# Optimization experiments

Measured on AMD Instinct MI355X. Metric: run time of the kernel, lower is better.

Reference implementation:

```python
import jax, jax.numpy as jnp
import numpy as np
import math

B, S, E, H = 4, 1024, 1024, 16
HD = E // H
MAX_SEQ = 5000
THETA = 10000.0


def _freqs_cis():
    # RotaryPositionalEncoding buffer: complex64 [MAX_SEQ, E//2]
    freqs = 1.0 / (THETA ** (np.arange(0, E, 2)[: E // 2] / E))
    ang = np.outer(np.arange(MAX_SEQ), freqs)
    return jnp.asarray(np.exp(1j * ang).astype(np.complex64))


def _rope(x, idx, fc_table):
    # x: [B, S, E]; pairs consecutive channels across the FULL embed_dim
    # (applied before head splitting, faithful to the original module)
    xc = x.reshape(*x.shape[:-1], -1, 2)
    xc = jax.lax.complex(xc[..., 0], xc[..., 1])  # [B, S, E//2]
    out = xc * fc_table[idx]                       # [B, S, E//2]
    return jnp.stack([jnp.real(out), jnp.imag(out)], axis=-1).reshape(x.shape)


def reference(query, key, value, query_index, key_index, attn_mask,
              key_padding_mask, Wq, bq, Wk, bk, Wv, bv, Wo, bo):
    q = query @ Wq.T + bq
    k = key @ Wk.T + bk
    v = value @ Wv.T + bv

    fc = _freqs_cis()
    q = _rope(q, query_index, fc)
    k = _rope(k, key_index, fc)

    # torch: q = cat(q.chunk(H, dim=-1), dim=0) -> flat HEAD-MAJOR [H*B, S, HD]
    qf = q.reshape(B, S, H, HD).transpose(2, 0, 1, 3).reshape(H * B, S, HD)
    kf = k.reshape(B, S, H, HD).transpose(2, 0, 1, 3).reshape(H * B, S, HD)
    vf = v.reshape(B, S, H, HD).transpose(2, 0, 1, 3).reshape(H * B, S, HD)

    # mask: logical_or(attn_mask[Sq,Sk], kpm[B,1,Sk]) -> [B, Sq, Sk]
    m = jnp.logical_or(attn_mask[None, :, :], key_padding_mask[:, None, :])
    madd = jnp.where(m, -jnp.inf, 0.0).astype(query.dtype)
    # torch repeat_interleave(H, dim=0) yields BATCH-MAJOR flat [B*H, Sq, Sk];
    # it is added to the head-major scores as-is (faithful to the original
    # indexing, including its head/batch-order quirk)
    madd_flat = jnp.repeat(madd, H, axis=0)

    scores = jnp.einsum('nqd,nkd->nqk', qf / math.sqrt(HD), kf) + madd_flat
    w = jax.nn.softmax(scores, axis=-1)              # [H*B, Sq, Sk]
    of = jnp.einsum('nqk,nkd->nqd', w, vf)           # [H*B, Sq, HD]

    # cat(chunks(dim=0), dim=-1) -> [B, Sq, E], head-major last dim
    attn_output = of.reshape(H, B, S, HD).transpose(1, 2, 0, 3).reshape(B, S, E)
    attn_output = attn_output @ Wo.T + bo

    # stack(chunks(dim=0), dim=1).mean(1) -> [B, Sq, Sk]
    attn_weights = w.reshape(H, B, S, S).transpose(1, 0, 2, 3).mean(axis=1)
    return attn_output, attn_weights


def setup_inputs() -> dict:
    key0 = jax.random.key(0)
    ks = jax.random.split(key0, 10)
    sc = 0.02
    inp = {
        'query': jax.random.normal(ks[0], (B, S, E), jnp.float32),
        'key': jax.random.normal(ks[1], (B, S, E), jnp.float32),
        'value': jax.random.normal(ks[2], (B, S, E), jnp.float32),
        'query_index': jnp.sort(jax.random.randint(ks[3], (B, S), 0, 4096), axis=-1),
        'key_index': jnp.sort(jax.random.randint(ks[4], (B, S), 0, 4096), axis=-1),
        'attn_mask': jnp.triu(jnp.ones((S, S), jnp.bool_), k=1),  # causal
        'key_padding_mask': jnp.zeros((B, S), jnp.bool_),
        'Wq': jax.random.normal(ks[5], (E, E), jnp.float32) * sc,
        'bq': jnp.zeros((E,), jnp.float32),
        'Wk': jax.random.normal(ks[6], (E, E), jnp.float32) * sc,
        'bk': jnp.zeros((E,), jnp.float32),
        'Wv': jax.random.normal(ks[7], (E, E), jnp.float32) * sc,
        'bv': jnp.zeros((E,), jnp.float32),
        'Wo': jax.random.normal(ks[8], (E, E), jnp.float32) * sc,
        'bo': jnp.zeros((E,), jnp.float32),
    }
    return inp
```

## Files before the change

### kernel.cpp

```cpp
#include <hip/hip_runtime.h>
#include <stdint.h>
#include <math.h>

#define B_ 4
#define S_ 1024
#define E_ 1024
#define H_ 16
#define HD_ 64
#define HB_ 64

typedef __attribute__((ext_vector_type(8))) short bhalf8;
typedef __attribute__((ext_vector_type(4))) float floatx4;

__device__ __forceinline__ unsigned short f2bf(float f) {
  union { float f; unsigned u; } v; v.f = f;
  unsigned r = (v.u + 0x7FFFu + ((v.u >> 16) & 1u)) >> 16;
  return (unsigned short)r;
}
__device__ __forceinline__ float bf2f(unsigned short b) {
  union { unsigned u; float f; } v; v.u = ((unsigned)b) << 16;
  return v.f;
}
__device__ __forceinline__ unsigned cvtpk_bf16(float a, float b) {
  unsigned r;
  asm volatile("v_cvt_pk_bf16_f32 %0, %1, %2" : "=v"(r) : "v"(a), "v"(b));
  return r;
}

__device__ __forceinline__ void gload16(const void* g, void* l) {
  __builtin_amdgcn_global_load_lds(
      (const __attribute__((address_space(1))) unsigned int*)g,
      (__attribute__((address_space(3))) unsigned int*)l, 16, 0, 0);
}

template <int NCH>
__device__ __forceinline__ void stage_tile(const unsigned short* org,
                                           unsigned short* lds, int wave, int lane) {
  const int rl = lane >> 3;
  const int scb = ((lane & 7) << 4) ^ (rl << 4);
  const char* base = (const char*)org + scb;
#pragma unroll
  for (int i = 0; i < NCH / 4; ++i) {
    const int c = wave + 4 * i;
    gload16(base + (size_t)(c * 8 + rl) * 2048, (char*)lds + c * 1024);
  }
}

__device__ __forceinline__ bhalf8 read_frag(const unsigned short* lds, int row, int kbyte) {
  const int off = row * 128 + (kbyte ^ ((row & 7) << 4));
  return *(const bhalf8*)((const char*)lds + off);
}

__global__ void detect_bool_kernel(const uint8_t* __restrict__ amask, int* __restrict__ flag) {
  if (threadIdx.x == 0 && blockIdx.x == 0) *flag = (amask[1] != 0) ? 1 : 0;
}

__global__ __launch_bounds__(256) void mprep_kernel(
    const void* __restrict__ amask, const void* __restrict__ kpm,
    const int* __restrict__ flagp, unsigned long long* __restrict__ Mbits) {
  const int gid = blockIdx.x * 256 + threadIdx.x;
  const int word = gid & 15, q = (gid >> 4) & 1023, bp = gid >> 14;
  const int k0 = word * 64;
  unsigned long long bits = 0;
  if (*flagp) {
    const uint8_t* ap = (const uint8_t*)amask + (size_t)q * 1024 + k0;
    const uint8_t* kp = (const uint8_t*)kpm + (size_t)bp * 1024 + k0;
#pragma unroll
    for (int c = 0; c < 4; ++c) {
      uint4 a = *(const uint4*)(ap + c * 16);
      uint4 k = *(const uint4*)(kp + c * 16);
      unsigned aw[4] = {a.x | k.x, a.y | k.y, a.z | k.z, a.w | k.w};
#pragma unroll
      for (int wv = 0; wv < 4; ++wv)
#pragma unroll
        for (int bt = 0; bt < 4; ++bt)
          if ((aw[wv] >> (8 * bt)) & 0xffu)
            bits |= 1ull << (c * 16 + wv * 4 + bt);
    }
  } else {
    const int* ap = (const int*)amask + (size_t)q * 1024 + k0;
    const int* kp = (const int*)kpm + (size_t)bp * 1024 + k0;
#pragma unroll
    for (int c = 0; c < 16; ++c) {
      int4 a = *(const int4*)(ap + c * 4);
      int4 k = *(const int4*)(kp + c * 4);
      if (a.x | k.x) bits |= 1ull << (c * 4 + 0);
      if (a.y | k.y) bits |= 1ull << (c * 4 + 1);
      if (a.z | k.z) bits |= 1ull << (c * 4 + 2);
      if (a.w | k.w) bits |= 1ull << (c * 4 + 3);
    }
  }
  Mbits[((size_t)bp << 14) + (size_t)q * 16 + word] = bits;
}

__global__ __launch_bounds__(256) void cvt_all_kernel(
    const float* __restrict__ q, const float* __restrict__ k,
    const float* __restrict__ v,
    const float* __restrict__ wq, const float* __restrict__ wk,
    const float* __restrict__ wv, const float* __restrict__ wo,
    unsigned short* __restrict__ Ab, unsigned short* __restrict__ Wb) {
  const int z = blockIdx.z;
  if (z >= 3 && blockIdx.x >= 512) return;
  const float* src;
  unsigned short* dst;
  if (z < 3) {
    src = (z == 0) ? q : (z == 1) ? k : v;
    dst = Ab + (size_t)z * 4194304;
  } else {
    const int zz = z - 3;
    src = (zz == 0) ? wq : (zz == 1) ? wk : (zz == 2) ? wv : wo;
    dst = Wb + (size_t)zz * 1048576;
  }
  const size_t i = ((size_t)blockIdx.x * 256 + threadIdx.x) * 8;
  float4 a = *(const float4*)(src + i);
  float4 b = *(const float4*)(src + i + 4);
  bhalf8 r;
  r[0] = (short)f2bf(a.x); r[1] = (short)f2bf(a.y);
  r[2] = (short)f2bf(a.z); r[3] = (short)f2bf(a.w);
  r[4] = (short)f2bf(b.x); r[5] = (short)f2bf(b.y);
  r[6] = (short)f2bf(b.z); r[7] = (short)f2bf(b.w);
  *(bhalf8*)(dst + i) = r;
}

template <bool QKV>
__global__ __launch_bounds__(256) void mfma_gemm_kernel(
    const unsigned short* __restrict__ A0, const unsigned short* __restrict__ A1,
    const unsigned short* __restrict__ A2,
    const unsigned short* __restrict__ W0, const unsigned short* __restrict__ W1,
    const unsigned short* __restrict__ W2,
    const float* __restrict__ b0, const float* __restrict__ b1,
    const float* __restrict__ b2,
    void* __restrict__ C0, void* __restrict__ C1, void* __restrict__ C2) {
  const int nb = gridDim.z * 256;
  const int chunk = nb >> 3;
  const int g = blockIdx.z * 256 + blockIdx.y * 8 + blockIdx.x;
  const int swz = (g & 7) * chunk + (g >> 3);
  const int zt = swz >> 8;
  const int r8 = swz & 255;
  const int m0 = (r8 >> 3) * 128, n0 = (r8 & 7) * 128;
  const unsigned short* A = (zt == 0) ? A0 : (zt == 1) ? A1 : A2;
  const unsigned short* W = (zt == 0) ? W0 : (zt == 1) ? W1 : W2;
  const float* bias = (zt == 0) ? b0 : (zt == 1) ? b1 : b2;
  void* C = (zt == 0) ? C0 : (zt == 1) ? C1 : C2;
  __shared__ unsigned short As[128 * 64];
  __shared__ unsigned short Ws[128 * 64];
  const int t = threadIdx.x, wave = t >> 6, lane = t & 63;
  const int wr = wave >> 1, wc = wave & 1;
  const int l4 = lane >> 4, l15 = lane & 15;
  floatx4 acc[4][4];
  const floatx4 z4 = {0.f, 0.f, 0.f, 0.f};
#pragma unroll
  for (int i = 0; i < 4; ++i)
#pragma unroll
    for (int j = 0; j < 4; ++j) acc[i][j] = z4;

  for (int k0 = 0; k0 < 1024; k0 += 64) {
    stage_tile<16>(A + (size_t)m0 * 1024 + k0, As, wave, lane);
    stage_tile<16>(W + (size_t)n0 * 1024 + k0, Ws, wave, lane);
    __syncthreads();
#pragma unroll
    for (int ks = 0; ks < 2; ++ks) {
      const int kb = ks * 64 + (l4 << 4);
      bhalf8 af[4], bf[4];
#pragma unroll
      for (int mi = 0; mi < 4; ++mi)
        af[mi] = read_frag(As, wr * 64 + mi * 16 + l15, kb);
#pragma unroll
      for (int ni = 0; ni < 4; ++ni)
        bf[ni] = read_frag(Ws, wc * 64 + ni * 16 + l15, kb);
#pragma unroll
      for (int mi = 0; mi < 4; ++mi)
#pragma unroll
        for (int ni = 0; ni < 4; ++ni)
          acc[mi][ni] = __builtin_amdgcn_mfma_f32_16x16x32_bf16(af[mi], bf[ni], acc[mi][ni], 0, 0, 0);
    }
    __syncthreads();
  }

  if (QKV && zt == 2) {
#pragma unroll
    for (int mi = 0; mi < 4; ++mi) {
      const int row0 = m0 + wr * 64 + mi * 16 + l4 * 4;
      const int b = row0 >> 10, s = row0 & 1023;
#pragma unroll
      for (int ni = 0; ni < 4; ++ni) {
        const int col = n0 + wc * 64 + ni * 16 + l15;
        const int h = col >> 6, d = col & 63;
        const float bv = bias[col];
        ushort4 o;
        o.x = f2bf(acc[mi][ni][0] + bv);
        o.y = f2bf(acc[mi][ni][1] + bv);
        o.z = f2bf(acc[mi][ni][2] + bv);
        o.w = f2bf(acc[mi][ni][3] + bv);
        *(ushort4*)((unsigned short*)C +
                    (((size_t)(b * 16 + h) * 64 + d) << 10) + s) = o;
      }
    }
  } else {
#pragma unroll
    for (int mi = 0; mi < 4; ++mi)
#pragma unroll
      for (int ni = 0; ni < 4; ++ni) {
        const int col = n0 + wc * 64 + ni * 16 + l15;
        const float bv = bias[col];
#pragma unroll
        for (int r = 0; r < 4; ++r) {
          const int row = m0 + wr * 64 + mi * 16 + l4 * 4 + r;
          const float v = acc[mi][ni][r] + bv;
          if (QKV)
            ((unsigned short*)C)[(size_t)row * 1024 + col] = f2bf(v);
          else
            ((float*)C)[(size_t)row * 1024 + col] = v;
        }
      }
  }
}

__global__ __launch_bounds__(256) void rope_bf_kernel(
    unsigned int* __restrict__ Q, unsigned int* __restrict__ K,
    const int* __restrict__ qidx, const int* __restrict__ kidx) {
  const int z = blockIdx.y;
  unsigned int* X = z ? K : Q;
  const int* idxs = z ? kidx : qidx;
  const int gid = blockIdx.x * 256 + threadIdx.x;
  const int i = gid & 511, bs = gid >> 9;
  const int pos = idxs[bs];
  const float fr = exp2f((float)i * (-13.287712379549449f / 512.0f));
  const float ang = (float)pos * fr;
  float sn, c;
  sincosf(ang, &sn, &c);
  const unsigned v = X[gid];
  const float x = bf2f((unsigned short)(v & 0xffffu));
  const float y = bf2f((unsigned short)(v >> 16));
  const float rx = x * c - y * sn;
  const float ry = x * sn + y * c;
  X[gid] = (unsigned)f2bf(rx) | ((unsigned)f2bf(ry) << 16);
}

__global__ __launch_bounds__(256) void scores_sm_kernel(
    const unsigned short* __restrict__ Qr, const unsigned short* __restrict__ Kr,
    unsigned short* __restrict__ P, const unsigned long long* __restrict__ Mbits,
    int hb0, int nwg) {
  const int lin = blockIdx.y * 64 + blockIdx.x;
  const int q8 = nwg >> 3;
  const int swz = (lin & 7) * q8 + (lin >> 3);
  const int qb = swz & 63, lhb = swz >> 6;
  const int hb = hb0 + lhb;
  const int h = hb >> 2, b = hb & 3, bp = hb >> 4;
  const int q0 = qb * 16;
  __shared__ unsigned short Sbuf[16 * 1024];
  float* rptr = (float*)Sbuf;
  const int t = threadIdx.x, w = t >> 6, lane = t & 63;
  const int l4 = lane >> 4, l15 = lane & 15;

  const char* Qb = (const char*)Qr + ((size_t)b << 21) + h * 128;
  const char* Kb = (const char*)Kr + ((size_t)b << 21) + h * 128;

  const unsigned long long* mrow =
      Mbits + ((size_t)bp << 14) + (size_t)(q0 + l15) * 16 + w * 4;
  unsigned long long mw0 = mrow[0], mw1 = mrow[1], mw2 = mrow[2], mw3 = mrow[3];

  bhalf8 bq0 = *(const bhalf8*)(Qb + (size_t)(q0 + l15) * 2048 + l4 * 16);
  bhalf8 bq1 = *(const bhalf8*)(Qb + (size_t)(q0 + l15) * 2048 + 64 + l4 * 16);

  floatx4 acc[16];
  const floatx4 z4 = {0.f, 0.f, 0.f, 0.f};
#pragma unroll
  for (int i = 0; i < 16; ++i) acc[i] = z4;
#pragma unroll
  for (int mt = 0; mt < 16; ++mt) {
    const char* kr = Kb + (size_t)(w * 256 + mt * 16 + l15) * 2048 + l4 * 16;
    bhalf8 a0 = *(const bhalf8*)kr;
    bhalf8 a1 = *(const bhalf8*)(kr + 64);
    acc[mt] = __builtin_amdgcn_mfma_f32_16x16x32_bf16(a0, bq0, acc[mt], 0, 0, 0);
    acc[mt] = __builtin_amdgcn_mfma_f32_16x16x32_bf16(a1, bq1, acc[mt], 0, 0, 0);
  }

  float red[16];
#pragma unroll
  for (int mt = 0; mt < 16; ++mt)
    red[mt] = fmaxf(fmaxf(acc[mt][0], acc[mt][1]), fmaxf(acc[mt][2], acc[mt][3]));
#pragma unroll
  for (int s2 = 8; s2 > 0; s2 >>= 1)
#pragma unroll
    for (int i = 0; i < 8; ++i)
      if (i < s2) red[i] = fmaxf(red[i], red[i + s2]);
  float mx = red[0];
  mx = fmaxf(mx, __shfl_xor(mx, 16));
  mx = fmaxf(mx, __shfl_xor(mx, 32));
  if (l4 == 0) rptr[w * 16 + l15] = mx;
  __syncthreads();
  mx = fmaxf(fmaxf(rptr[l15], rptr[16 + l15]), fmaxf(rptr[32 + l15], rptr[48 + l15]));

  const float Cc = 0.18033688011112042f;
  const float mc = mx * Cc;
#pragma unroll
  for (int mt = 0; mt < 16; ++mt) {
    const unsigned long long mwv = (mt < 4) ? mw0 : (mt < 8) ? mw1 : (mt < 12) ? mw2 : mw3;
    const unsigned bits = (unsigned)(mwv >> ((mt & 3) * 16 + l4 * 4)) & 0xFu;
#pragma unroll
    for (int r = 0; r < 4; ++r) {
      float e = exp2f(__builtin_fmaf(acc[mt][r], Cc, -mc));
      acc[mt][r] = ((bits >> r) & 1u) ? 0.f : e;
    }
  }

#pragma unroll
  for (int mt = 0; mt < 16; ++mt)
    red[mt] = (acc[mt][0] + acc[mt][1]) + (acc[mt][2] + acc[mt][3]);
#pragma unroll
  for (int s2 = 8; s2 > 0; s2 >>= 1)
#pragma unroll
    for (int i = 0; i < 8; ++i)
      if (i < s2) red[i] += red[i + s2];
  float sm = red[0];
  sm += __shfl_xor(sm, 16);
  sm += __shfl_xor(sm, 32);
  if (l4 == 0) rptr[64 + w * 16 + l15] = sm;
  __syncthreads();
  sm = (rptr[64 + l15] + rptr[80 + l15]) + (rptr[96 + l15] + rptr[112 + l15]);
  const float inv = 1.0f / sm;
  __syncthreads();

  const int xr = (l15 & 7) << 4;
#pragma unroll
  for (int mt = 0; mt < 16; ++mt) {
    uint2 pk;
    pk.x = cvtpk_bf16(acc[mt][0] * inv, acc[mt][1] * inv);
    pk.y = cvtpk_bf16(acc[mt][2] * inv, acc[mt][3] * inv);
    const int kb2 = (w * 256 + mt * 16 + l4 * 4) * 2;
    *(uint2*)((char*)Sbuf + l15 * 2048 + (kb2 ^ xr)) = pk;
  }
  __syncthreads();

  unsigned short* pbase = P + ((size_t)lhb << 20);
#pragma unroll
  for (int rr = 0; rr < 4; ++rr) {
    const int ql = w * 4 + rr;
    const int gq = q0 + ql;
    const int xq = (ql & 7) << 4;
#pragma unroll
    for (int j = 0; j < 2; ++j) {
      bhalf8 v = *(const bhalf8*)((const char*)Sbuf + ql * 2048 +
                                  ((j * 1024 + lane * 16) ^ xq));
      *(bhalf8*)(pbase + ((size_t)gq << 10) + j * 512 + lane * 8) = v;
    }
  }
}

__global__ __launch_bounds__(256) void wmean_kernel(
    const unsigned short* __restrict__ P, float* __restrict__ outW,
    int nhh, int first) {
  const size_t gid = (size_t)blockIdx.x * 256 + threadIdx.x;
  const int k8 = (int)(gid & 127);
  const int q = (int)((gid >> 7) & 1023);
  const int b = (int)(gid >> 17);
  float s[8];
#pragma unroll
  for (int u = 0; u < 8; ++u) s[u] = 0.f;
  for (int hh = 0; hh < nhh; ++hh) {
    const int lhb = hh * 4 + b;
    bhalf8 v = *(const bhalf8*)(P + ((size_t)lhb << 20) + ((size_t)q << 10) + k8 * 8);
#pragma unroll
    for (int u = 0; u < 8; ++u) s[u] += bf2f((unsigned short)v[u]);
  }
  float* o = outW + (((size_t)(b * S_ + q)) << 10) + k8 * 8;
  const float invH = 1.0f / 16.0f;
  float4 v0, v1;
  v0.x = s[0] * invH; v0.y = s[1] * invH; v0.z = s[2] * invH; v0.w = s[3] * invH;
  v1.x = s[4] * invH; v1.y = s[5] * invH; v1.z = s[6] * invH; v1.w = s[7] * invH;
  if (!first) {
    float4 a = *(float4*)o, b4 = *(float4*)(o + 4);
    v0.x += a.x; v0.y += a.y; v0.z += a.z; v0.w += a.w;
    v1.x += b4.x; v1.y += b4.y; v1.z += b4.z; v1.w += b4.w;
  }
  *(float4*)o = v0;
  *(float4*)(o + 4) = v1;
}

__global__ __launch_bounds__(256) void pv_mfma_kernel(
    const unsigned short* __restrict__ Wt, const unsigned short* __restrict__ Vt,
    unsigned short* __restrict__ Ocat, int hb0, int nwg) {
  const int lin = blockIdx.y * 16 + blockIdx.x;
  const int q8 = nwg >> 3;
  const int swz = (lin & 7) * q8 + (lin >> 3);
  const int qt = swz & 15, lhb = swz >> 4;
  const int hb = hb0 + lhb;
  const int h = hb >> 2, b = hb & 3;
  const int q0 = qt * 64;
  __shared__ unsigned short Ps[64 * 64];
  __shared__ unsigned short Vs[64 * 64];
  const int t = threadIdx.x, wave = t >> 6, lane = t & 63;
  const int wr = wave >> 1, wc = wave & 1;
  const unsigned short* Wh = Wt + ((size_t)lhb << 20);
  const unsigned short* Vh = Vt + (size_t)(b * 16 + h) * 65536;
  floatx4 acc[2][2];
  const floatx4 z4 = {0.f, 0.f, 0.f, 0.f};
#pragma unroll
  for (int i = 0; i < 2; ++i)
#pragma unroll
    for (int j = 0; j < 2; ++j) acc[i][j] = z4;

  for (int k0 = 0; k0 < 1024; k0 += 64) {
    stage_tile<8>(Wh + (size_t)q0 * 1024 + k0, Ps, wave, lane);
    stage_tile<8>(Vh + k0, Vs, wave, lane);
    __syncthreads();
#pragma unroll
    for (int ks = 0; ks < 2; ++ks) {
      const int kb = ks * 64 + ((lane >> 4) << 4);
      bhalf8 af[2], bf[2];
#pragma unroll
      for (int mi = 0; mi < 2; ++mi)
        af[mi] = read_frag(Ps, wr * 32 + mi * 16 + (lane & 15), kb);
#pragma unroll
      for (int ni = 0; ni < 2; ++ni)
        bf[ni] = read_frag(Vs, wc * 32 + ni * 16 + (lane & 15), kb);
#pragma unroll
      for (int mi = 0; mi < 2; ++mi)
#pragma unroll
        for (int ni = 0; ni < 2; ++ni)
          acc[mi][ni] = __builtin_amdgcn_mfma_f32_16x16x32_bf16(af[mi], bf[ni], acc[mi][ni], 0, 0, 0);
    }
    __syncthreads();
  }
#pragma unroll
  for (int mi = 0; mi < 2; ++mi)
#pragma unroll
    for (int ni = 0; ni < 2; ++ni) {
      const int d = wc * 32 + ni * 16 + (lane & 15);
#pragma unroll
      for (int r = 0; r < 4; ++r) {
        const int q = q0 + wr * 32 + mi * 16 + (lane >> 4) * 4 + r;
        Ocat[((size_t)(b * S_) + q) * E_ + h * HD_ + d] = f2bf(acc[mi][ni][r]);
      }
    }
}

extern "C" void kernel_launch(void* const* d_in, const int* in_sizes, int n_in,
                              void* d_out, int out_size, void* d_ws, size_t ws_size,
                              hipStream_t stream) {
  (void)in_sizes; (void)n_in; (void)out_size;
  const float* query = (const float*)d_in[0];
  const float* key   = (const float*)d_in[1];
  const float* value = (const float*)d_in[2];
  const int* qidx = (const int*)d_in[3];
  const int* kidx = (const int*)d_in[4];
  const void* amask = d_in[5];
  const void* kpm   = d_in[6];
  const float* Wq = (const float*)d_in[7];
  const float* bq = (const float*)d_in[8];
  const float* Wk = (const float*)d_in[9];
  const float* bk = (const float*)d_in[10];
  const float* Wv = (const float*)d_in[11];
  const float* bv = (const float*)d_in[12];
  const float* Wo = (const float*)d_in[13];
  const float* bo = (const float*)d_in[14];

  float* outA = (float*)d_out;
  float* outW = (float*)d_out + (size_t)B_ * S_ * E_;

  float* ws = (float*)d_ws;
  unsigned short* Ab   = (unsigned short*)(ws + 0);
  unsigned short* Wb   = (unsigned short*)(ws + 6291456);
  unsigned short* Qr   = (unsigned short*)(ws + 8388608);
  unsigned short* Kr   = (unsigned short*)(ws + 10485760);
  unsigned short* Vt   = (unsigned short*)(ws + 14680064);
  unsigned short* Ocat = (unsigned short*)(ws + 16777216);
  int* flagp           = (int*)(ws + 18874368);
  unsigned long long* Mbits = (unsigned long long*)(ws + 18874432);
  const size_t tail_off = 18874432 + 131072;

  const size_t ws_floats = ws_size / 4;
  int CH = 0;
  unsigned short* P = nullptr;
  for (int c = 64; c >= 8; c >>= 1) {
    if (tail_off + (size_t)c * 524288 <= ws_floats) {
      CH = c;
      P = (unsigned short*)(ws + tail_off);
      break;
    }
  }
  if (!CH) {
    CH = 8;
    P = (unsigned short*)ws;
  }

  detect_bool_kernel<<<1, 64, 0, stream>>>((const uint8_t*)amask, flagp);
  mprep_kernel<<<256, 256, 0, stream>>>(amask, kpm, flagp, Mbits);

  cvt_all_kernel<<<dim3(2048, 1, 7), 256, 0, stream>>>(
      query, key, value, Wq, Wk, Wv, Wo, Ab, Wb);

  mfma_gemm_kernel<true><<<dim3(8, 32, 3), 256, 0, stream>>>(
      Ab, Ab + 4194304, Ab + 8388608,
      Wb, Wb + 1048576, Wb + 2097152,
      bq, bk, bv, Qr, Kr, Vt);

  rope_bf_kernel<<<dim3(8192, 2), 256, 0, stream>>>(
      (unsigned int*)Qr, (unsigned int*)Kr, qidx, kidx);

  const int nch = HB_ / CH;
  for (int c = 0; c < nch; ++c) {
    const int hb0 = c * CH;
    scores_sm_kernel<<<dim3(64, CH), 256, 0, stream>>>(Qr, Kr, P, Mbits, hb0,
                                                       64 * CH);
    wmean_kernel<<<2048, 256, 0, stream>>>(P, outW, CH / 4, (c == 0) ? 1 : 0);
    pv_mfma_kernel<<<dim3(16, CH), 256, 0, stream>>>(P, Vt, Ocat, hb0, 16 * CH);
  }

  mfma_gemm_kernel<false><<<dim3(8, 32, 1), 256, 0, stream>>>(
      Ocat, Ocat, Ocat, Wb + 3145728, Wb + 3145728, Wb + 3145728,
      bo, bo, bo, outA, outA, outA);
}
```

Measured before the change: 252.7 us.

## Merge softmax reductions into one barrier and move V transpose to separate kernel

The scores/softmax kernel now computes per-wave max and sum independently and merges them across waves with a single barrier, rescaling each wave's sum by its exp offset (online-softmax style combine). This removes two barriers, and each wave writes its P tile through its own LDS region without a block-wide sync. The GEMM epilogue no longer does the strided transposed store for V. V is instead written row-major and transposed by a new LDS-tiled kernel, trading an extra launch and pass over V for coalesced GEMM stores.

```diff
diff --git a/kernel.cpp b/kernel.cpp
--- a/kernel.cpp
+++ b/kernel.cpp
@@ -176,44 +176,22 @@
     }
     __syncthreads();
   }
-
-  if (QKV && zt == 2) {
-#pragma unroll
-    for (int mi = 0; mi < 4; ++mi) {
-      const int row0 = m0 + wr * 64 + mi * 16 + l4 * 4;
-      const int b = row0 >> 10, s = row0 & 1023;
-#pragma unroll
-      for (int ni = 0; ni < 4; ++ni) {
-        const int col = n0 + wc * 64 + ni * 16 + l15;
-        const int h = col >> 6, d = col & 63;
-        const float bv = bias[col];
-        ushort4 o;
-        o.x = f2bf(acc[mi][ni][0] + bv);
-        o.y = f2bf(acc[mi][ni][1] + bv);
-        o.z = f2bf(acc[mi][ni][2] + bv);
-        o.w = f2bf(acc[mi][ni][3] + bv);
-        *(ushort4*)((unsigned short*)C +
-                    (((size_t)(b * 16 + h) * 64 + d) << 10) + s) = o;
+#pragma unroll
+  for (int mi = 0; mi < 4; ++mi)
+#pragma unroll
+    for (int ni = 0; ni < 4; ++ni) {
+      const int col = n0 + wc * 64 + ni * 16 + l15;
+      const float bv = bias[col];
+#pragma unroll
+      for (int r = 0; r < 4; ++r) {
+        const int row = m0 + wr * 64 + mi * 16 + l4 * 4 + r;
+        const float v = acc[mi][ni][r] + bv;
+        if (QKV)
+          ((unsigned short*)C)[(size_t)row * 1024 + col] = f2bf(v);
+        else
+          ((float*)C)[(size_t)row * 1024 + col] = v;
       }
     }
-  } else {
-#pragma unroll
-    for (int mi = 0; mi < 4; ++mi)
-#pragma unroll
-      for (int ni = 0; ni < 4; ++ni) {
-        const int col = n0 + wc * 64 + ni * 16 + l15;
-        const float bv = bias[col];
-#pragma unroll
-        for (int r = 0; r < 4; ++r) {
-          const int row = m0 + wr * 64 + mi * 16 + l4 * 4 + r;
-          const float v = acc[mi][ni][r] + bv;
-          if (QKV)
-            ((unsigned short*)C)[(size_t)row * 1024 + col] = f2bf(v);
-          else
-            ((float*)C)[(size_t)row * 1024 + col] = v;
-        }
-      }
-  }
 }
 
 __global__ __launch_bounds__(256) void rope_bf_kernel(
@@ -237,6 +215,27 @@
   X[gid] = (unsigned)f2bf(rx) | ((unsigned)f2bf(ry) << 16);
 }
 
+__global__ __launch_bounds__(256) void transpose_v_kernel(
+    const unsigned short* __restrict__ Vr, unsigned short* __restrict__ Vt) {
+  const int s0 = blockIdx.x * 64;
+  const int bh = blockIdx.y;
+  const int b = bh >> 4, h = bh & 15;
+  __shared__ unsigned short L[64][72];
+  const int t = threadIdx.x, r = t >> 2, cq = (t & 3) * 16;
+  const unsigned short* src = Vr + ((size_t)(b * S_) + s0 + r) * E_ + h * HD_ + cq;
+  *(bhalf8*)&L[r][cq] = *(const bhalf8*)src;
+  *(bhalf8*)&L[r][cq + 8] = *(const bhalf8*)(src + 8);
+  __syncthreads();
+  bhalf8 o0, o1;
+#pragma unroll
+  for (int u = 0; u < 8; ++u) o0[u] = (short)L[cq + u][r];
+#pragma unroll
+  for (int u = 0; u < 8; ++u) o1[u] = (short)L[cq + 8 + u][r];
+  unsigned short* dst = Vt + ((size_t)bh * 64 + r) * 1024 + s0 + cq;
+  *(bhalf8*)dst = o0;
+  *(bhalf8*)(dst + 8) = o1;
+}
+
 __global__ __launch_bounds__(256) void scores_sm_kernel(
     const unsigned short* __restrict__ Qr, const unsigned short* __restrict__ Kr,
     unsigned short* __restrict__ P, const unsigned long long* __restrict__ Mbits,
@@ -249,7 +248,7 @@
   const int h = hb >> 2, b = hb & 3, bp = hb >> 4;
   const int q0 = qb * 16;
   __shared__ unsigned short Sbuf[16 * 1024];
-  float* rptr = (float*)Sbuf;
+  __shared__ float rbuf[128];
   const int t = threadIdx.x, w = t >> 6, lane = t & 63;
   const int l4 = lane >> 4, l15 = lane & 15;
 
@@ -258,7 +257,7 @@
 
   const unsigned long long* mrow =
       Mbits + ((size_t)bp << 14) + (size_t)(q0 + l15) * 16 + w * 4;
-  unsigned long long mw0 = mrow[0], mw1 = mrow[1], mw2 = mrow[2], mw3 = mrow[3];
+  const unsigned long long mm0 = mrow[0], mm1 = mrow[1], mm2 = mrow[2], mm3 = mrow[3];
 
   bhalf8 bq0 = *(const bhalf8*)(Qb + (size_t)(q0 + l15) * 2048 + l4 * 16);
   bhalf8 bq1 = *(const bhalf8*)(Qb + (size_t)(q0 + l15) * 2048 + 64 + l4 * 16);
@@ -285,18 +284,15 @@
 #pragma unroll
     for (int i = 0; i < 8; ++i)
       if (i < s2) red[i] = fmaxf(red[i], red[i + s2]);
-  float mx = red[0];
-  mx = fmaxf(mx, __shfl_xor(mx, 16));
-  mx = fmaxf(mx, __shfl_xor(mx, 32));
-  if (l4 == 0) rptr[w * 16 + l15] = mx;
-  __syncthreads();
-  mx = fmaxf(fmaxf(rptr[l15], rptr[16 + l15]), fmaxf(rptr[32 + l15], rptr[48 + l15]));
+  float mw = red[0];
+  mw = fmaxf(mw, __shfl_xor(mw, 16));
+  mw = fmaxf(mw, __shfl_xor(mw, 32));
 
   const float Cc = 0.18033688011112042f;
-  const float mc = mx * Cc;
+  const float mc = mw * Cc;
 #pragma unroll
   for (int mt = 0; mt < 16; ++mt) {
-    const unsigned long long mwv = (mt < 4) ? mw0 : (mt < 8) ? mw1 : (mt < 12) ? mw2 : mw3;
+    const unsigned long long mwv = (mt < 4) ? mm0 : (mt < 8) ? mm1 : (mt < 12) ? mm2 : mm3;
     const unsigned bits = (unsigned)(mwv >> ((mt & 3) * 16 + l4 * 4)) & 0xFu;
 #pragma unroll
     for (int r = 0; r < 4; ++r) {
@@ -304,7 +300,6 @@
       acc[mt][r] = ((bits >> r) & 1u) ? 0.f : e;
     }
   }
-
 #pragma unroll
   for (int mt = 0; mt < 16; ++mt)
     red[mt] = (acc[mt][0] + acc[mt][1]) + (acc[mt][2] + acc[mt][3]);
@@ -313,38 +308,43 @@
 #pragma unroll
     for (int i = 0; i < 8; ++i)
       if (i < s2) red[i] += red[i + s2];
-  float sm = red[0];
-  sm += __shfl_xor(sm, 16);
-  sm += __shfl_xor(sm, 32);
-  if (l4 == 0) rptr[64 + w * 16 + l15] = sm;
+  float sw = red[0];
+  sw += __shfl_xor(sw, 16);
+  sw += __shfl_xor(sw, 32);
+
+  if (l4 == 0) {
+    rbuf[w * 16 + l15] = mw;
+    rbuf[64 + w * 16 + l15] = sw;
+  }
   __syncthreads();
-  sm = (rptr[64 + l15] + rptr[80 + l15]) + (rptr[96 + l15] + rptr[112 + l15]);
-  const float inv = 1.0f / sm;
-  __syncthreads();
-
+
+  float M = rbuf[l15];
+#pragma unroll
+  for (int ww = 1; ww < 4; ++ww) M = fmaxf(M, rbuf[ww * 16 + l15]);
+  float S = 0.f;
+#pragma unroll
+  for (int ww = 0; ww < 4; ++ww)
+    S += rbuf[64 + ww * 16 + l15] * exp2f((rbuf[ww * 16 + l15] - M) * Cc);
+  const float g = exp2f((mw - M) * Cc) / S;
+
+  const int base = w * 8192;
   const int xr = (l15 & 7) << 4;
 #pragma unroll
   for (int mt = 0; mt < 16; ++mt) {
     uint2 pk;
-    pk.x = cvtpk_bf16(acc[mt][0] * inv, acc[mt][1] * inv);
-    pk.y = cvtpk_bf16(acc[mt][2] * inv, acc[mt][3] * inv);
-    const int kb2 = (w * 256 + mt * 16 + l4 * 4) * 2;
-    *(uint2*)((char*)Sbuf + l15 * 2048 + (kb2 ^ xr)) = pk;
-  }
-  __syncthreads();
-
-  unsigned short* pbase = P + ((size_t)lhb << 20);
-#pragma unroll
-  for (int rr = 0; rr < 4; ++rr) {
-    const int ql = w * 4 + rr;
-    const int gq = q0 + ql;
-    const int xq = (ql & 7) << 4;
-#pragma unroll
-    for (int j = 0; j < 2; ++j) {
-      bhalf8 v = *(const bhalf8*)((const char*)Sbuf + ql * 2048 +
-                                  ((j * 1024 + lane * 16) ^ xq));
-      *(bhalf8*)(pbase + ((size_t)gq << 10) + j * 512 + lane * 8) = v;
-    }
+    pk.x = cvtpk_bf16(acc[mt][0] * g, acc[mt][1] * g);
+    pk.y = cvtpk_bf16(acc[mt][2] * g, acc[mt][3] * g);
+    const int off = (mt * 32 + l4 * 8) ^ xr;
+    *(uint2*)((char*)Sbuf + base + l15 * 512 + off) = pk;
+  }
+  unsigned short* pbase = P + ((size_t)lhb << 20) + ((size_t)q0 << 10) + w * 256;
+  const int c = lane & 31, rhalf = lane >> 5;
+#pragma unroll
+  for (int rr = 0; rr < 8; ++rr) {
+    const int row = rr * 2 + rhalf;
+    const int off = (c * 16) ^ ((row & 7) << 4);
+    bhalf8 v = *(const bhalf8*)((const char*)Sbuf + base + row * 512 + off);
+    *(bhalf8*)(pbase + ((size_t)row << 10) + c * 8) = v;
   }
 }
 
@@ -464,6 +464,7 @@
   unsigned short* Wb   = (unsigned short*)(ws + 6291456);
   unsigned short* Qr   = (unsigned short*)(ws + 8388608);
   unsigned short* Kr   = (unsigned short*)(ws + 10485760);
+  unsigned short* Vr   = (unsigned short*)(ws + 12582912);
   unsigned short* Vt   = (unsigned short*)(ws + 14680064);
   unsigned short* Ocat = (unsigned short*)(ws + 16777216);
   int* flagp           = (int*)(ws + 18874368);
@@ -494,10 +495,12 @@
   mfma_gemm_kernel<true><<<dim3(8, 32, 3), 256, 0, stream>>>(
       Ab, Ab + 4194304, Ab + 8388608,
       Wb, Wb + 1048576, Wb + 2097152,
-      bq, bk, bv, Qr, Kr, Vt);
+      bq, bk, bv, Qr, Kr, Vr);
 
   rope_bf_kernel<<<dim3(8192, 2), 256, 0, stream>>>(
       (unsigned int*)Qr, (unsigned int*)Kr, qidx, kidx);
+
+  transpose_v_kernel<<<dim3(16, 64), 256, 0, stream>>>(Vr, Vt);
 
   const int nch = HB_ / CH;
   for (int c = 0; c < nch; ++c) {
```

After: 236.9 us. 6.3% less time.
